# Optimization experiments

Hardware: AMD Instinct MI355X
Metric: run time of the kernel (lower is better)

The kernel has to match this reference:

```python
import jax, jax.numpy as jnp
import numpy as np

E = 1024   # embed_dim
H = 16     # num_heads
NQ = 8     # ffn_dim == n_qubits
B, S = 2, 2048


def setup_inputs() -> dict:
    key = jax.random.key(0)
    ks = jax.random.split(key, 8)
    g = lambda k, sh, sc=1.0: jax.random.normal(k, sh, jnp.float32) * sc
    return {
        "x": g(ks[0], (B, S, E)),
        "w_qkv": g(ks[1], (3 * E, E), 0.02),      # nn.Linear(E, 3E, bias=False).weight
        "w_comb": g(ks[2], (E, E), 0.02),          # combine Linear weight
        "b_comb": jnp.zeros((E,), jnp.float32),
        "gamma1": jnp.ones((E,), jnp.float32),     # norm1
        "beta1": jnp.zeros((E,), jnp.float32),
        "gamma2": jnp.ones((E,), jnp.float32),     # norm2
        "beta2": jnp.zeros((E,), jnp.float32),
        "theta": g(ks[3], (NQ,)),                  # trainable RY angles
        "w1": g(ks[4], (1, NQ), 0.3),              # linear1 weight [1, n_qubits]
        "b1": jnp.zeros((1,), jnp.float32),
    }


def _layernorm(x, g, b, eps=1e-5):
    m = jnp.mean(x, axis=-1, keepdims=True)
    v = jnp.var(x, axis=-1, keepdims=True)
    return (x - m) * jax.lax.rsqrt(v + eps) * g + b


def reference(x, w_qkv, w_comb, b_comb, gamma1, beta1, gamma2, beta2, theta, w1, b1):
    Bx, Sx, Em = x.shape
    dk = Em // H
    # ---- attention ----
    qkv = (x @ w_qkv.T).reshape(Bx, Sx, 3, H, dk)
    q = jnp.transpose(qkv[:, :, 0], (0, 2, 1, 3))  # [B,H,S,dk]
    k = jnp.transpose(qkv[:, :, 1], (0, 2, 1, 3))
    v = jnp.transpose(qkv[:, :, 2], (0, 2, 1, 3))
    scores = jnp.einsum('bhqd,bhkd->bhqk', q, k) / jnp.sqrt(jnp.float32(dk))
    probs = jax.nn.softmax(scores, axis=-1)        # dropout = identity (eval)
    out = jnp.einsum('bhqk,bhkd->bhqd', probs, v)
    out = jnp.transpose(out, (0, 2, 1, 3)).reshape(Bx, Sx, Em)
    attn = out @ w_comb.T + b_comb
    x1 = _layernorm(x + attn, gamma1, beta1)
    # ---- quantum FFN: RX(x_i) encode, RY(theta_i), <Z_i> = cos(theta_i)*cos(x_i) ----
    z = jnp.cos(x1[..., :theta.shape[0]]) * jnp.cos(theta)  # [B,S,NQ]
    ffn = z @ w1.T + b1                                      # [B,S,1], broadcasts
    return _layernorm(x1 + ffn, gamma2, beta2)
```

## Files before the change

kernel.cpp:

```cpp
#include <hip/hip_runtime.h>
#include <hip/hip_bf16.h>
#include <math.h>

typedef __bf16 bf16;
typedef bf16 bf16x8 __attribute__((ext_vector_type(8)));
typedef bf16 bf16x4 __attribute__((ext_vector_type(4)));
typedef float f32x4 __attribute__((ext_vector_type(4)));
typedef unsigned int u32;

#define EMB 1024
#define NH 16
#define DK 64
#define SEQ 2048
#define NB 2
#define NTOK (NB*SEQ)

#define QSCALE 0.18033688011112043f

#if defined(__has_builtin)
#if __has_builtin(__builtin_amdgcn_exp2f)
#define EXP2(x) __builtin_amdgcn_exp2f(x)
#else
#define EXP2(x) exp2f(x)
#endif
#else
#define EXP2(x) exp2f(x)
#endif

__device__ __forceinline__ void gl_lds16(const void* g, void* l) {
    __builtin_amdgcn_global_load_lds(
        (const __attribute__((address_space(1))) u32*)g,
        (__attribute__((address_space(3))) u32*)l, 16, 0, 0);
}

#define SWZ(row, colblk) (((row)*64) + ((((colblk) ^ ((row)&7)))*8))

#define PSTR 72

__device__ __forceinline__ void xcd_remap(int gx, int* bx, int* by) {
    int gy  = gridDim.y;
    int nwg = gx * gy;
    int wg  = *by * gx + *bx;
    int per = nwg >> 3;
    int s   = (wg & 7) * per + (wg >> 3);
    *bx = s % gx;
    *by = s / gx;
}

__global__ __launch_bounds__(256) void convert3(
    const float* __restrict__ s0, const float* __restrict__ s1,
    const float* __restrict__ s2,
    bf16* __restrict__ d0, bf16* __restrict__ d1, bf16* __restrict__ d2)
{
    const float* src; bf16* dst; int n;
    switch (blockIdx.y) {
        case 0:  src = s0; dst = d0; n = NTOK*EMB;  break;
        case 1:  src = s1; dst = d1; n = 3*EMB*EMB; break;
        default: src = s2; dst = d2; n = EMB*EMB;   break;
    }
    int i = (blockIdx.x * 256 + threadIdx.x) * 8;
    if (i + 7 < n) {
        float4 a = *(const float4*)(src + i);
        float4 b = *(const float4*)(src + i + 4);
        bf16x8 o;
        o[0] = (bf16)a.x; o[1] = (bf16)a.y; o[2] = (bf16)a.z; o[3] = (bf16)a.w;
        o[4] = (bf16)b.x; o[5] = (bf16)b.y; o[6] = (bf16)b.z; o[7] = (bf16)b.w;
        *(bf16x8*)(dst + i) = o;
    }
}

template<int MODE, int BM>
__global__ __launch_bounds__(256) void gemm_bt(
    const bf16* __restrict__ Aa, const bf16* __restrict__ Bb,
    bf16* __restrict__ qb, bf16* __restrict__ kb, bf16* __restrict__ vtb,
    float* __restrict__ outc, int Kdim)
{
    constexpr int MI = BM / 32;
    __shared__ __align__(16) bf16 At0[BM*64];
    __shared__ __align__(16) bf16 At1[BM*64];
    __shared__ __align__(16) bf16 Bt0[128*64];
    __shared__ __align__(16) bf16 Bt1[128*64];
    const int tid  = threadIdx.x;
    const int w    = tid >> 6, lane = tid & 63;
    const int quad = lane >> 4, l15 = lane & 15;
    const int wr   = w >> 1,   wc  = w & 1;
    int bx = blockIdx.x, by = blockIdx.y;
    xcd_remap(gridDim.x, &bx, &by);
    const int m0 = by * BM, n0 = bx * 128;
    const int lrow = lane >> 3;
    const int lswz = ((lane & 7) ^ lrow) * 8;

    f32x4 acc[MI][4] = {};

    auto stageAB = [&](int k0, bf16* At, bf16* Bt) {
        #pragma unroll
        for (int i = 0; i < MI; ++i) {
            int r = w*(BM/4) + i*8 + lrow;
            gl_lds16(Aa + (size_t)(m0 + r)*Kdim + k0 + lswz, At + (w*(BM/4) + i*8)*64);
        }
        #pragma unroll
        for (int i = 0; i < 4; ++i) {
            int r = w*32 + i*8 + lrow;
            gl_lds16(Bb + (size_t)(n0 + r)*Kdim + k0 + lswz, Bt + (w*32 + i*8)*64);
        }
    };

    auto computeAB = [&](const bf16* At, const bf16* Bt) {
        #pragma unroll
        for (int kk = 0; kk < 2; ++kk) {
            bf16x8 a[MI], b[4];
            #pragma unroll
            for (int i = 0; i < MI; ++i)
                a[i] = *(const bf16x8*)(At + SWZ(wr*(BM/2) + i*16 + l15, 4*kk + quad));
            #pragma unroll
            for (int j = 0; j < 4; ++j)
                b[j] = *(const bf16x8*)(Bt + SWZ(wc*64 + j*16 + l15, 4*kk + quad));
            __builtin_amdgcn_s_setprio(1);
            #pragma unroll
            for (int i = 0; i < MI; ++i)
                #pragma unroll
                for (int j = 0; j < 4; ++j)
                    acc[i][j] = __builtin_amdgcn_mfma_f32_16x16x32_bf16(a[i], b[j], acc[i][j], 0, 0, 0);
            __builtin_amdgcn_s_setprio(0);
        }
    };

    const int NT2 = Kdim >> 7;
    stageAB(0, At0, Bt0);
    for (int t2 = 0; t2 < NT2; ++t2) {
        __syncthreads();
        stageAB(t2*128 + 64, At1, Bt1);
        computeAB(At0, Bt0);
        __syncthreads();
        if (t2 + 1 < NT2)
            stageAB(t2*128 + 128, At0, Bt0);
        computeAB(At1, Bt1);
    }

    for (int i = 0; i < MI; ++i) for (int j = 0; j < 4; ++j) {
        int rb  = m0 + wr*(BM/2) + i*16 + quad*4;
        int col = n0 + wc*64 + j*16 + l15;
        if (MODE == 0) {
            int c = col >> 10, h = (col >> 6) & 15, d = col & 63;
            int b_ = rb >> 11, s = rb & 2047;
            int bh = b_*NH + h;
            if (c == 2) {
                bf16 tmp[4] __attribute__((aligned(8)));
                for (int r = 0; r < 4; ++r) tmp[r] = (bf16)acc[i][j][r];
                *(ushort4*)(vtb + ((size_t)bh*DK + d)*SEQ + s) = *(ushort4*)tmp;
            } else if (c == 0) {
                for (int r = 0; r < 4; ++r)
                    qb[((size_t)bh*SEQ + s + r)*DK + d] = (bf16)(acc[i][j][r] * QSCALE);
            } else {
                for (int r = 0; r < 4; ++r)
                    kb[((size_t)bh*SEQ + s + r)*DK + d] = (bf16)acc[i][j][r];
            }
        } else {
            for (int r = 0; r < 4; ++r)
                outc[(size_t)(rb + r)*EMB + col] = acc[i][j][r];
        }
    }
}

__global__ __launch_bounds__(512) void attn_kernel(
    const bf16* __restrict__ q, const bf16* __restrict__ k,
    const bf16* __restrict__ vt, bf16* __restrict__ out)
{
    __shared__ __align__(16) bf16 QP[8*16*PSTR];
    __shared__ __align__(16) bf16 Kt0[64*64];
    __shared__ __align__(16) bf16 Kt1[64*64];
    __shared__ __align__(16) bf16 Vt0[64*64];
    __shared__ __align__(16) bf16 Vt1[64*64];

    const int tid  = threadIdx.x;
    const int w    = tid >> 6, lane = tid & 63;
    const int quad = lane >> 4, l15 = lane & 15;
    int qt = blockIdx.x, bh = blockIdx.y;
    xcd_remap(gridDim.x, &qt, &bh);
    const int lrow = lane >> 3;
    const int lswz = ((lane & 7) ^ lrow) * 8;

    for (int i = 0; i < 2; ++i) {
        int r = w*16 + i*8 + lrow;
        gl_lds16(q + ((size_t)bh*SEQ + qt*128 + r)*DK + lswz, QP + (w*16 + i*8)*64);
    }
    asm volatile("s_waitcnt vmcnt(0)" ::: "memory");

    bf16x8 qf[2];
    for (int kk = 0; kk < 2; ++kk)
        qf[kk] = *(const bf16x8*)(QP + SWZ(w*16 + l15, 4*kk + quad));

    bf16* Pw = QP + w * 16 * PSTR;

    f32x4 O[4] = {};
    float psum = 0.f;

    auto stage_kv = [&](int kt, bf16* Kb, bf16* Vb) {
        int r = w*8 + lrow;
        gl_lds16(k  + ((size_t)bh*SEQ + kt*64 + r)*DK + lswz, Kb + (w*8)*64);
        gl_lds16(vt + ((size_t)bh*DK + r)*SEQ + kt*64 + lswz, Vb + (w*8)*64);
    };

    auto compute = [&](const bf16* Kb, const bf16* Vb) {
        f32x4 sc[4] = {};
        for (int kk = 0; kk < 2; ++kk) {
            bf16x8 kf[4];
            for (int j = 0; j < 4; ++j)
                kf[j] = *(const bf16x8*)(Kb + SWZ(j*16 + l15, 4*kk + quad));
            __builtin_amdgcn_s_setprio(1);
            for (int j = 0; j < 4; ++j)
                sc[j] = __builtin_amdgcn_mfma_f32_16x16x32_bf16(kf[j], qf[kk], sc[j], 0, 0, 0);
            __builtin_amdgcn_s_setprio(0);
        }
        for (int j = 0; j < 4; ++j) {
            bf16x4 pk;
            for (int r = 0; r < 4; ++r) {
                float p = EXP2(sc[j][r]);
                psum += p;
                pk[r] = (bf16)p;
            }
            *(bf16x4*)(Pw + l15*PSTR + j*16 + quad*4) = pk;
        }
        asm volatile("s_waitcnt lgkmcnt(0)" ::: "memory");
        for (int kk = 0; kk < 2; ++kk) {
            bf16x8 vb[4];
            for (int j = 0; j < 4; ++j)
                vb[j] = *(const bf16x8*)(Vb + SWZ(j*16 + l15, 4*kk + quad));
            bf16x8 a = *(const bf16x8*)(Pw + l15*PSTR + kk*32 + quad*8);
            __builtin_amdgcn_s_setprio(1);
            for (int j = 0; j < 4; ++j)
                O[j] = __builtin_amdgcn_mfma_f32_16x16x32_bf16(a, vb[j], O[j], 0, 0, 0);
            __builtin_amdgcn_s_setprio(0);
        }
    };

    stage_kv(0, Kt0, Vt0);
    for (int kt2 = 0; kt2 < SEQ/128; ++kt2) {
        __syncthreads();
        stage_kv(2*kt2 + 1, Kt1, Vt1);
        compute(Kt0, Vt0);
        __syncthreads();
        if (kt2 + 1 < SEQ/128)
            stage_kv(2*kt2 + 2, Kt0, Vt0);
        compute(Kt1, Vt1);
    }

    float s = psum;
    s += __shfl_xor(s, 16, 64);
    s += __shfl_xor(s, 32, 64);
    float inv[4];
    for (int r = 0; r < 4; ++r)
        inv[r] = 1.f / __shfl(s, quad*4 + r, 64);

    const int b_ = bh >> 4, h = bh & 15;
    for (int j = 0; j < 4; ++j)
        for (int r = 0; r < 4; ++r) {
            int t   = b_*SEQ + qt*128 + w*16 + quad*4 + r;
            int col = h*DK + j*16 + l15;
            out[(size_t)t*EMB + col] = (bf16)(O[j][r] * inv[r]);
        }
}

__global__ __launch_bounds__(256) void ln_kernel(
    const float* __restrict__ x, const float* __restrict__ comb,
    const float* __restrict__ bcomb,
    const float* __restrict__ g1, const float* __restrict__ be1,
    const float* __restrict__ g2, const float* __restrict__ be2,
    const float* __restrict__ theta, const float* __restrict__ w1v,
    const float* __restrict__ b1v, float* __restrict__ out)
{
    const int w    = threadIdx.x >> 6, lane = threadIdx.x & 63;
    const int t    = blockIdx.x * 4 + w;

    float r[4][4];
    float s = 0.f, ss = 0.f;
    #pragma unroll
    for (int c = 0; c < 4; ++c) {
        int e = c*256 + lane*4;
        float4 xv = *(const float4*)(x    + (size_t)t*EMB + e);
        float4 cv = *(const float4*)(comb + (size_t)t*EMB + e);
        float4 bv = *(const float4*)(bcomb + e);
        r[c][0] = xv.x + cv.x + bv.x; r[c][1] = xv.y + cv.y + bv.y;
        r[c][2] = xv.z + cv.z + bv.z; r[c][3] = xv.w + cv.w + bv.w;
        #pragma unroll
        for (int i = 0; i < 4; ++i) { s += r[c][i]; ss += r[c][i]*r[c][i]; }
    }
    #pragma unroll
    for (int m = 1; m < 64; m <<= 1) { s += __shfl_xor(s, m, 64); ss += __shfl_xor(ss, m, 64); }
    float mean = s * (1.f/1024.f);
    float var  = ss * (1.f/1024.f) - mean*mean;
    float inv  = rsqrtf(var + 1e-5f);

    float x1[4][4];
    #pragma unroll
    for (int c = 0; c < 4; ++c) {
        int e = c*256 + lane*4;
        #pragma unroll
        for (int i = 0; i < 4; ++i)
            x1[c][i] = (r[c][i] - mean)*inv*g1[e+i] + be1[e+i];
    }

    float pf = 0.f;
    if (lane < 2) {
        #pragma unroll
        for (int i = 0; i < 4; ++i) {
            int e = lane*4 + i;
            pf += cosf(x1[0][i]) * cosf(theta[e]) * w1v[e];
        }
    }
    pf += __shfl_xor(pf, 1, 64);
    float f = __shfl(pf, 0, 64) + b1v[0];

    float s2 = 0.f, ss2 = 0.f;
    #pragma unroll
    for (int c = 0; c < 4; ++c)
        #pragma unroll
        for (int i = 0; i < 4; ++i) {
            float v2 = x1[c][i] + f; s2 += v2; ss2 += v2*v2;
        }
    #pragma unroll
    for (int m = 1; m < 64; m <<= 1) { s2 += __shfl_xor(s2, m, 64); ss2 += __shfl_xor(ss2, m, 64); }
    float mean2 = s2 * (1.f/1024.f);
    float var2  = ss2 * (1.f/1024.f) - mean2*mean2;
    float inv2  = rsqrtf(var2 + 1e-5f);

    #pragma unroll
    for (int c = 0; c < 4; ++c) {
        int e = c*256 + lane*4;
        float4 ov;
        ov.x = ((x1[c][0] + f) - mean2)*inv2*g2[e+0] + be2[e+0];
        ov.y = ((x1[c][1] + f) - mean2)*inv2*g2[e+1] + be2[e+1];
        ov.z = ((x1[c][2] + f) - mean2)*inv2*g2[e+2] + be2[e+2];
        ov.w = ((x1[c][3] + f) - mean2)*inv2*g2[e+3] + be2[e+3];
        *(float4*)(out + (size_t)t*EMB + e) = ov;
    }
}

extern "C" void kernel_launch(void* const* d_in, const int* in_sizes, int n_in,
                              void* d_out, int out_size, void* d_ws, size_t ws_size,
                              hipStream_t stream)
{
    const float* x      = (const float*)d_in[0];
    const float* w_qkv  = (const float*)d_in[1];
    const float* w_comb = (const float*)d_in[2];
    const float* b_comb = (const float*)d_in[3];
    const float* g1     = (const float*)d_in[4];
    const float* be1    = (const float*)d_in[5];
    const float* g2     = (const float*)d_in[6];
    const float* be2    = (const float*)d_in[7];
    const float* theta  = (const float*)d_in[8];
    const float* w1v    = (const float*)d_in[9];
    const float* b1v    = (const float*)d_in[10];
    float* out = (float*)d_out;

    char* ws = (char*)d_ws;
    bf16*  xb     = (bf16*)(ws);
    bf16*  wqkvb  = (bf16*)(ws + ( 8u<<20));
    bf16*  wcombb = (bf16*)(ws + (14u<<20));
    bf16*  qb     = (bf16*)(ws + (16u<<20));
    bf16*  kb     = (bf16*)(ws + (24u<<20));
    bf16*  vtb    = (bf16*)(ws + (32u<<20));
    bf16*  attn   = (bf16*)(ws + (40u<<20));
    float* comb   = (float*)(ws + (16u<<20));

    convert3<<<dim3(2048, 3), 256, 0, stream>>>(x, w_qkv, w_comb, xb, wqkvb, wcombb);

    gemm_bt<0,128><<<dim3(3*EMB/128, NTOK/128), 256, 0, stream>>>(
        xb, wqkvb, qb, kb, vtb, nullptr, EMB);
    attn_kernel<<<dim3(SEQ/128, NB*NH), 512, 0, stream>>>(qb, kb, vtb, attn);
    gemm_bt<1,64><<<dim3(EMB/128, NTOK/64), 256, 0, stream>>>(
        attn, wcombb, nullptr, nullptr, nullptr, comb, EMB);
    ln_kernel<<<NTOK/4, 256, 0, stream>>>(x, comb, b_comb, g1, be1, g2, be2,
                                          theta, w1v, b1v, out);
}
```

Before: 197.1 us.

## Process 32 query rows per wave in attention to reuse K/V fragments

The attention kernel moves from 8 waves of 16 query rows to 4 waves of 32 query rows per 128-row block, so each wave computes two row tiles. Every K and V fragment read from LDS now feeds two MFMAs instead of one, which halves LDS read traffic per MFMA. The cost is higher register pressure and fewer waves per block to hide latency. Each wave also issues twice as many staging loads.

```diff
diff --git a/kernel.cpp b/kernel.cpp
--- a/kernel.cpp
+++ b/kernel.cpp
@@ -162,11 +162,11 @@
     }
 }
 
-__global__ __launch_bounds__(512) void attn_kernel(
+__global__ __launch_bounds__(256) void attn_kernel(
     const bf16* __restrict__ q, const bf16* __restrict__ k,
     const bf16* __restrict__ vt, bf16* __restrict__ out)
 {
-    __shared__ __align__(16) bf16 QP[8*16*PSTR];
+    __shared__ __align__(16) bf16 QP[4*32*PSTR];
     __shared__ __align__(16) bf16 Kt0[64*64];
     __shared__ __align__(16) bf16 Kt1[64*64];
     __shared__ __align__(16) bf16 Vt0[64*64];
@@ -180,56 +180,73 @@
     const int lrow = lane >> 3;
     const int lswz = ((lane & 7) ^ lrow) * 8;
 
-    for (int i = 0; i < 2; ++i) {
-        int r = w*16 + i*8 + lrow;
-        gl_lds16(q + ((size_t)bh*SEQ + qt*128 + r)*DK + lswz, QP + (w*16 + i*8)*64);
+    for (int i = 0; i < 4; ++i) {
+        int r = w*32 + i*8 + lrow;
+        gl_lds16(q + ((size_t)bh*SEQ + qt*128 + r)*DK + lswz, QP + (w*32 + i*8)*64);
     }
     asm volatile("s_waitcnt vmcnt(0)" ::: "memory");
 
-    bf16x8 qf[2];
-    for (int kk = 0; kk < 2; ++kk)
-        qf[kk] = *(const bf16x8*)(QP + SWZ(w*16 + l15, 4*kk + quad));
-
-    bf16* Pw = QP + w * 16 * PSTR;
-
-    f32x4 O[4] = {};
-    float psum = 0.f;
+    bf16x8 qf[2][2];
+    for (int rt = 0; rt < 2; ++rt)
+        for (int kk = 0; kk < 2; ++kk)
+            qf[rt][kk] = *(const bf16x8*)(QP + SWZ(w*32 + rt*16 + l15, 4*kk + quad));
+
+    bf16* Pw = QP + w * 32 * PSTR;
+
+    f32x4 O[2][4] = {};
+    float psum[2] = {};
 
     auto stage_kv = [&](int kt, bf16* Kb, bf16* Vb) {
-        int r = w*8 + lrow;
-        gl_lds16(k  + ((size_t)bh*SEQ + kt*64 + r)*DK + lswz, Kb + (w*8)*64);
-        gl_lds16(vt + ((size_t)bh*DK + r)*SEQ + kt*64 + lswz, Vb + (w*8)*64);
+        #pragma unroll
+        for (int i = 0; i < 2; ++i) {
+            int r = w*16 + i*8 + lrow;
+            gl_lds16(k  + ((size_t)bh*SEQ + kt*64 + r)*DK + lswz, Kb + (w*16 + i*8)*64);
+            gl_lds16(vt + ((size_t)bh*DK + r)*SEQ + kt*64 + lswz, Vb + (w*16 + i*8)*64);
+        }
     };
 
     auto compute = [&](const bf16* Kb, const bf16* Vb) {
-        f32x4 sc[4] = {};
+        f32x4 sc[2][4] = {};
         for (int kk = 0; kk < 2; ++kk) {
             bf16x8 kf[4];
+            #pragma unroll
             for (int j = 0; j < 4; ++j)
                 kf[j] = *(const bf16x8*)(Kb + SWZ(j*16 + l15, 4*kk + quad));
             __builtin_amdgcn_s_setprio(1);
-            for (int j = 0; j < 4; ++j)
-                sc[j] = __builtin_amdgcn_mfma_f32_16x16x32_bf16(kf[j], qf[kk], sc[j], 0, 0, 0);
+            #pragma unroll
+            for (int j = 0; j < 4; ++j) {
+                sc[0][j] = __builtin_amdgcn_mfma_f32_16x16x32_bf16(kf[j], qf[0][kk], sc[0][j], 0, 0, 0);
+                sc[1][j] = __builtin_amdgcn_mfma_f32_16x16x32_bf16(kf[j], qf[1][kk], sc[1][j], 0, 0, 0);
+            }
             __builtin_amdgcn_s_setprio(0);
         }
-        for (int j = 0; j < 4; ++j) {
-            bf16x4 pk;
-            for (int r = 0; r < 4; ++r) {
-                float p = EXP2(sc[j][r]);
-                psum += p;
-                pk[r] = (bf16)p;
+        #pragma unroll
+        for (int rt = 0; rt < 2; ++rt)
+            #pragma unroll
+            for (int j = 0; j < 4; ++j) {
+                bf16x4 pk;
+                #pragma unroll
+                for (int r = 0; r < 4; ++r) {
+                    float p = EXP2(sc[rt][j][r]);
+                    psum[rt] += p;
+                    pk[r] = (bf16)p;
+                }
+                *(bf16x4*)(Pw + (rt*16 + l15)*PSTR + j*16 + quad*4) = pk;
             }
-            *(bf16x4*)(Pw + l15*PSTR + j*16 + quad*4) = pk;
-        }
         asm volatile("s_waitcnt lgkmcnt(0)" ::: "memory");
         for (int kk = 0; kk < 2; ++kk) {
             bf16x8 vb[4];
+            #pragma unroll
             for (int j = 0; j < 4; ++j)
                 vb[j] = *(const bf16x8*)(Vb + SWZ(j*16 + l15, 4*kk + quad));
-            bf16x8 a = *(const bf16x8*)(Pw + l15*PSTR + kk*32 + quad*8);
+            bf16x8 a0 = *(const bf16x8*)(Pw + (     l15)*PSTR + kk*32 + quad*8);
+            bf16x8 a1 = *(const bf16x8*)(Pw + (16 + l15)*PSTR + kk*32 + quad*8);
             __builtin_amdgcn_s_setprio(1);
-            for (int j = 0; j < 4; ++j)
-                O[j] = __builtin_amdgcn_mfma_f32_16x16x32_bf16(a, vb[j], O[j], 0, 0, 0);
+            #pragma unroll
+            for (int j = 0; j < 4; ++j) {
+                O[0][j] = __builtin_amdgcn_mfma_f32_16x16x32_bf16(a0, vb[j], O[0][j], 0, 0, 0);
+                O[1][j] = __builtin_amdgcn_mfma_f32_16x16x32_bf16(a1, vb[j], O[1][j], 0, 0, 0);
+            }
             __builtin_amdgcn_s_setprio(0);
         }
     };
@@ -245,20 +262,28 @@
         compute(Kt1, Vt1);
     }
 
-    float s = psum;
-    s += __shfl_xor(s, 16, 64);
-    s += __shfl_xor(s, 32, 64);
-    float inv[4];
-    for (int r = 0; r < 4; ++r)
-        inv[r] = 1.f / __shfl(s, quad*4 + r, 64);
+    float inv[2][4];
+    #pragma unroll
+    for (int rt = 0; rt < 2; ++rt) {
+        float s = psum[rt];
+        s += __shfl_xor(s, 16, 64);
+        s += __shfl_xor(s, 32, 64);
+        #pragma unroll
+        for (int r = 0; r < 4; ++r)
+            inv[rt][r] = 1.f / __shfl(s, quad*4 + r, 64);
+    }
 
     const int b_ = bh >> 4, h = bh & 15;
-    for (int j = 0; j < 4; ++j)
-        for (int r = 0; r < 4; ++r) {
-            int t   = b_*SEQ + qt*128 + w*16 + quad*4 + r;
-            int col = h*DK + j*16 + l15;
-            out[(size_t)t*EMB + col] = (bf16)(O[j][r] * inv[r]);
-        }
+    #pragma unroll
+    for (int rt = 0; rt < 2; ++rt)
+        #pragma unroll
+        for (int j = 0; j < 4; ++j)
+            #pragma unroll
+            for (int r = 0; r < 4; ++r) {
+                int t   = b_*SEQ + qt*128 + w*32 + rt*16 + quad*4 + r;
+                int col = h*DK + j*16 + l15;
+                out[(size_t)t*EMB + col] = (bf16)(O[rt][j][r] * inv[rt][r]);
+            }
 }
 
 __global__ __launch_bounds__(256) void ln_kernel(
@@ -367,7 +392,7 @@
 
     gemm_bt<0,128><<<dim3(3*EMB/128, NTOK/128), 256, 0, stream>>>(
         xb, wqkvb, qb, kb, vtb, nullptr, EMB);
-    attn_kernel<<<dim3(SEQ/128, NB*NH), 512, 0, stream>>>(qb, kb, vtb, attn);
+    attn_kernel<<<dim3(SEQ/128, NB*NH), 256, 0, stream>>>(qb, kb, vtb, attn);
     gemm_bt<1,64><<<dim3(EMB/128, NTOK/64), 256, 0, stream>>>(
         attn, wcombb, nullptr, nullptr, nullptr, comb, EMB);
     ln_kernel<<<NTOK/4, 256, 0, stream>>>(x, comb, b_comb, g1, be1, g2, be2,
```

After: 206.1 us. 4.5% more time.

## Shrink attention tiles to 64 queries and 32-key steps with split K/V staging

Applied to the files above, without the earlier changes.

The attention kernel now uses 4 waves (256 threads) per block over 64 query rows instead of 8 waves over 128, doubling the grid. K is streamed in 32-row tiles while V is staged in 64-key tiles every other step, with separate double-buffered staging and a smaller P scratch stride. The aim is more blocks and lower LDS per block for better occupancy and latency hiding, at the cost of more K/V reloads per query and more barriers per key.

```diff
diff --git a/kernel.cpp b/kernel.cpp
--- a/kernel.cpp
+++ b/kernel.cpp
@@ -35,7 +35,7 @@
 
 #define SWZ(row, colblk) (((row)*64) + ((((colblk) ^ ((row)&7)))*8))
 
-#define PSTR 72
+#define PST 40
 
 __device__ __forceinline__ void xcd_remap(int gx, int* bx, int* by) {
     int gy  = gridDim.y;
@@ -162,13 +162,13 @@
     }
 }
 
-__global__ __launch_bounds__(512) void attn_kernel(
+__global__ __launch_bounds__(256) void attn_kernel(
     const bf16* __restrict__ q, const bf16* __restrict__ k,
     const bf16* __restrict__ vt, bf16* __restrict__ out)
 {
-    __shared__ __align__(16) bf16 QP[8*16*PSTR];
-    __shared__ __align__(16) bf16 Kt0[64*64];
-    __shared__ __align__(16) bf16 Kt1[64*64];
+    __shared__ __align__(16) bf16 QP[64*64];
+    __shared__ __align__(16) bf16 Kt0[32*64];
+    __shared__ __align__(16) bf16 Kt1[32*64];
     __shared__ __align__(16) bf16 Vt0[64*64];
     __shared__ __align__(16) bf16 Vt1[64*64];
 
@@ -182,7 +182,15 @@
 
     for (int i = 0; i < 2; ++i) {
         int r = w*16 + i*8 + lrow;
-        gl_lds16(q + ((size_t)bh*SEQ + qt*128 + r)*DK + lswz, QP + (w*16 + i*8)*64);
+        gl_lds16(q + ((size_t)bh*SEQ + qt*64 + r)*DK + lswz, QP + (w*16 + i*8)*64);
+    }
+    {
+        int r = w*8 + lrow;
+        gl_lds16(k + ((size_t)bh*SEQ + r)*DK + lswz, Kt0 + (w*8)*64);
+    }
+    for (int i = 0; i < 2; ++i) {
+        int r = w*16 + i*8 + lrow;
+        gl_lds16(vt + ((size_t)bh*DK + r)*SEQ + lswz, Vt0 + (w*16 + i*8)*64);
     }
     asm volatile("s_waitcnt vmcnt(0)" ::: "memory");
 
@@ -190,59 +198,70 @@
     for (int kk = 0; kk < 2; ++kk)
         qf[kk] = *(const bf16x8*)(QP + SWZ(w*16 + l15, 4*kk + quad));
 
-    bf16* Pw = QP + w * 16 * PSTR;
+    bf16* Pw = QP + w * 16 * PST;
 
     f32x4 O[4] = {};
     float psum = 0.f;
 
-    auto stage_kv = [&](int kt, bf16* Kb, bf16* Vb) {
+    auto stage_k = [&](int st, bf16* Kb) {
         int r = w*8 + lrow;
-        gl_lds16(k  + ((size_t)bh*SEQ + kt*64 + r)*DK + lswz, Kb + (w*8)*64);
-        gl_lds16(vt + ((size_t)bh*DK + r)*SEQ + kt*64 + lswz, Vb + (w*8)*64);
-    };
-
-    auto compute = [&](const bf16* Kb, const bf16* Vb) {
-        f32x4 sc[4] = {};
+        gl_lds16(k + ((size_t)bh*SEQ + st*32 + r)*DK + lswz, Kb + (w*8)*64);
+    };
+    auto stage_v = [&](int vp, bf16* Vb) {
+        #pragma unroll
+        for (int i = 0; i < 2; ++i) {
+            int r = w*16 + i*8 + lrow;
+            gl_lds16(vt + ((size_t)bh*DK + r)*SEQ + vp*64 + lswz, Vb + (w*16 + i*8)*64);
+        }
+    };
+
+    auto compute = [&](const bf16* Kb, const bf16* Vb, int h) {
+        f32x4 sc[2] = {};
+        #pragma unroll
         for (int kk = 0; kk < 2; ++kk) {
-            bf16x8 kf[4];
-            for (int j = 0; j < 4; ++j)
-                kf[j] = *(const bf16x8*)(Kb + SWZ(j*16 + l15, 4*kk + quad));
+            bf16x8 kf0 = *(const bf16x8*)(Kb + SWZ(     l15, 4*kk + quad));
+            bf16x8 kf1 = *(const bf16x8*)(Kb + SWZ(16 + l15, 4*kk + quad));
             __builtin_amdgcn_s_setprio(1);
-            for (int j = 0; j < 4; ++j)
-                sc[j] = __builtin_amdgcn_mfma_f32_16x16x32_bf16(kf[j], qf[kk], sc[j], 0, 0, 0);
+            sc[0] = __builtin_amdgcn_mfma_f32_16x16x32_bf16(kf0, qf[kk], sc[0], 0, 0, 0);
+            sc[1] = __builtin_amdgcn_mfma_f32_16x16x32_bf16(kf1, qf[kk], sc[1], 0, 0, 0);
             __builtin_amdgcn_s_setprio(0);
         }
-        for (int j = 0; j < 4; ++j) {
+        #pragma unroll
+        for (int j = 0; j < 2; ++j) {
             bf16x4 pk;
+            #pragma unroll
             for (int r = 0; r < 4; ++r) {
                 float p = EXP2(sc[j][r]);
                 psum += p;
                 pk[r] = (bf16)p;
             }
-            *(bf16x4*)(Pw + l15*PSTR + j*16 + quad*4) = pk;
+            *(bf16x4*)(Pw + l15*PST + j*16 + quad*4) = pk;
         }
         asm volatile("s_waitcnt lgkmcnt(0)" ::: "memory");
-        for (int kk = 0; kk < 2; ++kk) {
-            bf16x8 vb[4];
-            for (int j = 0; j < 4; ++j)
-                vb[j] = *(const bf16x8*)(Vb + SWZ(j*16 + l15, 4*kk + quad));
-            bf16x8 a = *(const bf16x8*)(Pw + l15*PSTR + kk*32 + quad*8);
-            __builtin_amdgcn_s_setprio(1);
-            for (int j = 0; j < 4; ++j)
-                O[j] = __builtin_amdgcn_mfma_f32_16x16x32_bf16(a, vb[j], O[j], 0, 0, 0);
-            __builtin_amdgcn_s_setprio(0);
-        }
-    };
-
-    stage_kv(0, Kt0, Vt0);
-    for (int kt2 = 0; kt2 < SEQ/128; ++kt2) {
+        bf16x8 a = *(const bf16x8*)(Pw + l15*PST + quad*8);
+        bf16x8 vb[4];
+        #pragma unroll
+        for (int j = 0; j < 4; ++j)
+            vb[j] = *(const bf16x8*)(Vb + SWZ(j*16 + l15, h*4 + quad));
+        __builtin_amdgcn_s_setprio(1);
+        #pragma unroll
+        for (int j = 0; j < 4; ++j)
+            O[j] = __builtin_amdgcn_mfma_f32_16x16x32_bf16(a, vb[j], O[j], 0, 0, 0);
+        __builtin_amdgcn_s_setprio(0);
+    };
+
+    const int NK2 = SEQ / 64;
+    for (int kt2 = 0; kt2 < NK2; ++kt2) {
+        const bf16* Vb = (kt2 & 1) ? Vt1 : Vt0;
         __syncthreads();
-        stage_kv(2*kt2 + 1, Kt1, Vt1);
-        compute(Kt0, Vt0);
+        stage_k(2*kt2 + 1, Kt1);
+        if (kt2 + 1 < NK2)
+            stage_v(kt2 + 1, (kt2 & 1) ? Vt0 : Vt1);
+        compute(Kt0, Vb, 0);
         __syncthreads();
-        if (kt2 + 1 < SEQ/128)
-            stage_kv(2*kt2 + 2, Kt0, Vt0);
-        compute(Kt1, Vt1);
+        if (kt2 + 1 < NK2)
+            stage_k(2*kt2 + 2, Kt0);
+        compute(Kt1, Vb, 1);
     }
 
     float s = psum;
@@ -255,7 +274,7 @@
     const int b_ = bh >> 4, h = bh & 15;
     for (int j = 0; j < 4; ++j)
         for (int r = 0; r < 4; ++r) {
-            int t   = b_*SEQ + qt*128 + w*16 + quad*4 + r;
+            int t   = b_*SEQ + qt*64 + w*16 + quad*4 + r;
             int col = h*DK + j*16 + l15;
             out[(size_t)t*EMB + col] = (bf16)(O[j][r] * inv[r]);
         }
@@ -367,7 +386,7 @@
 
     gemm_bt<0,128><<<dim3(3*EMB/128, NTOK/128), 256, 0, stream>>>(
         xb, wqkvb, qb, kb, vtb, nullptr, EMB);
-    attn_kernel<<<dim3(SEQ/128, NB*NH), 512, 0, stream>>>(qb, kb, vtb, attn);
+    attn_kernel<<<dim3(SEQ/64, NB*NH), 256, 0, stream>>>(qb, kb, vtb, attn);
     gemm_bt<1,64><<<dim3(EMB/128, NTOK/64), 256, 0, stream>>>(
         attn, wcombb, nullptr, nullptr, nullptr, comb, EMB);
     ln_kernel<<<NTOK/4, 256, 0, stream>>>(x, comb, b_comb, g1, be1, g2, be2,
```

Result: slower. 202.4 us (+2.7%).
